# Performance work log

Hardware: AMD Instinct MI355X
Metric: run time of the kernel (lower is better)

The kernel has to match this reference:

```python
import jax, jax.numpy as jnp
import numpy as np

NUM_CLASSES = 32
MAX_DET = 100        # max_detections
CONF = 0.25          # conf_threshold
IOU_THR = 0.45       # iou_threshold
BATCH = 64
ANCHORS = 8400


def setup_inputs() -> dict:
    key = jax.random.key(0)
    # raw YOLO head output [B, 4+num_classes, anchors]; uniform [0,1) so boxes
    # (normalized cx,cy,w,h) and class scores are in valid range.
    yolo_output = jax.random.uniform(key, (BATCH, 4 + NUM_CLASSES, ANCHORS), dtype=jnp.float32)
    return {"yolo_output": yolo_output}


def _iou_one_vs_all(box, boxes):
    # box: [4] (ymin,xmin,ymax,xmax); boxes: [A,4]
    y1 = jnp.maximum(box[0], boxes[:, 0])
    x1 = jnp.maximum(box[1], boxes[:, 1])
    y2 = jnp.minimum(box[2], boxes[:, 2])
    x2 = jnp.minimum(box[3], boxes[:, 3])
    inter = jnp.maximum(y2 - y1, 0.0) * jnp.maximum(x2 - x1, 0.0)
    area_a = (box[2] - box[0]) * (box[3] - box[1])
    area_b = (boxes[:, 2] - boxes[:, 0]) * (boxes[:, 3] - boxes[:, 1])
    union = area_a + area_b - inter
    return jnp.where(union > 0.0, inter / union, 0.0)


def _nms_one_image(boxes, classes, scores):
    # Greedy hard NMS, equivalent to tf.image.non_max_suppression followed by
    # gather + zero-pad to MAX_DET. `scores` already has sub-threshold anchors
    # masked to -1 (emulating boolean_mask by threshold).
    def step(sc, _):
        idx = jnp.argmax(sc)
        s = sc[idx]
        b = boxes[idx]
        c = classes[idx]
        ok = s > 0.0  # any remaining valid candidate?
        iou = _iou_one_vs_all(b, boxes)
        new_sc = jnp.where(iou > IOU_THR, -1.0, sc).at[idx].set(-1.0)
        sc = jnp.where(ok, new_sc, sc)
        out = (jnp.where(ok, b, 0.0), jnp.where(ok, c, 0.0), jnp.where(ok, s, 0.0), ok)
        return sc, out

    _, (sel_boxes, sel_classes, sel_scores, valid) = jax.lax.scan(
        step, scores, None, length=MAX_DET)
    num_det = jnp.sum(valid.astype(jnp.float32))
    return sel_boxes, sel_classes, sel_scores, num_det


def _forward(yolo_output):
    # [B, 36, A] -> [B, A, 36]
    t = jnp.transpose(yolo_output, (0, 2, 1))
    boxes_raw = t[..., :4]                      # cx, cy, w, h (normalized)
    class_scores = t[..., 4:]                   # [B, A, num_classes]
    best_scores = jnp.max(class_scores, axis=-1)
    best_classes = jax.lax.stop_gradient(
        jnp.argmax(class_scores, axis=-1).astype(jnp.float32))
    xc, yc, w, h = (boxes_raw[..., 0], boxes_raw[..., 1],
                    boxes_raw[..., 2], boxes_raw[..., 3])
    clip = lambda v: jnp.clip(v, 0.0, 1.0)
    # TF order: [ymin, xmin, ymax, xmax]
    corner = jnp.stack([clip(yc - h * 0.5), clip(xc - w * 0.5),
                        clip(yc + h * 0.5), clip(xc + w * 0.5)], axis=-1)
    # confidence threshold: mask out instead of boolean_mask (jit-friendly)
    masked_scores = jnp.where(best_scores >= CONF, best_scores, -1.0)
    det_boxes, det_classes, det_scores, num_det = jax.vmap(_nms_one_image)(
        corner, best_classes, masked_scores)
    return det_boxes, det_classes, det_scores, num_det


def reference(yolo_output):
    # Returns (detection_boxes [B,100,4], detection_classes [B,100],
    #          detection_scores [B,100], num_detections [B])
    return _forward(yolo_output)
```

## Files before the change

### kernel.cpp

```cpp
#include <hip/hip_runtime.h>

#define BATCH   64
#define CHANS   36
#define ANCH    8400
#define NCLS    32
#define MAXDET  100
#define CONF    0.25f
#define TPB     512
#define NW      (TPB / 64)
#define NLD     17
#define KEYMIN  0x3E800000u
#define NBUCK   2048
#define BUCK0   (0x3E800000u >> 13)
#define WCAP    256

typedef unsigned long long u64;
typedef unsigned int       u32;

__global__ __launch_bounds__(256) void yolo_prep(const float* __restrict__ in,
                                                 float4* __restrict__ wbox,
                                                 u64* __restrict__ wk64) {
#pragma clang fp contract(off)
    const int G = ANCH / 4;
    int g = blockIdx.x * 256 + threadIdx.x;
    if (g >= G) return;
    int b = blockIdx.y;
    const float4* p = (const float4*)(in + (size_t)b * (CHANS * ANCH));
    float4 xc = p[0 * G + g], yc = p[1 * G + g], ww = p[2 * G + g], hh = p[3 * G + g];
    float4 best = p[4 * G + g];
    uint4 bc = make_uint4(0, 0, 0, 0);
#pragma unroll
    for (int k = 1; k < NCLS; ++k) {
        float4 v = p[(4 + k) * G + g];
        if (v.x > best.x) { best.x = v.x; bc.x = k; }
        if (v.y > best.y) { best.y = v.y; bc.y = k; }
        if (v.z > best.z) { best.z = v.z; bc.z = k; }
        if (v.w > best.w) { best.w = v.w; bc.w = k; }
    }
    int a0 = b * ANCH + 4 * g;
    u64* wk = wk64 + (size_t)b * ANCH + 4 * g;
#define PREP_C(C, I)                                                      \
    {                                                                     \
        float Y1 = fminf(fmaxf(yc.C - hh.C * 0.5f, 0.f), 1.f);            \
        float X1 = fminf(fmaxf(xc.C - ww.C * 0.5f, 0.f), 1.f);            \
        float Y2 = fminf(fmaxf(yc.C + hh.C * 0.5f, 0.f), 1.f);            \
        float X2 = fminf(fmaxf(xc.C + ww.C * 0.5f, 0.f), 1.f);            \
        wbox[a0 + I] = make_float4(Y1, X1, Y2, X2);                       \
        int a_ = 4 * g + I;                                               \
        wk[I] = (best.C >= CONF)                                          \
            ? (((u64)__float_as_uint(best.C) << 32) |                     \
               ((u64)(16383 - a_) << 18) | (u64)(bc.C & 31u))             \
            : 0ull;                                                       \
    }
    PREP_C(x, 0) PREP_C(y, 1) PREP_C(z, 2) PREP_C(w, 3)
#undef PREP_C
}

__global__ __launch_bounds__(TPB) void yolo_nms(const float4* __restrict__ wbox,
                                                u64* __restrict__ wk64,
                                                float* __restrict__ out) {
#pragma clang fp contract(off)
    const double M = (double)0.45f + 0x1p-26;
    int b = blockIdx.x, t = threadIdx.x;
    const float4* bx = wbox + (size_t)b * ANCH;
    u64* gk = wk64 + (size_t)b * ANCH;

    __shared__ u32   hist[NBUCK];
    __shared__ int   cur[NBUCK];
    __shared__ u64   cKey[WCAP];
    __shared__ float4 cBox[WCAP];
    __shared__ float cAr[WCAP];
    __shared__ u64   SuppA[WCAP][4];
    __shared__ u64   SuppB[WCAP][4];
    __shared__ u64   Smask[4];
    __shared__ int   selTot;
    __shared__ u32   wvcnt[NW];
    __shared__ u32   wprd[NW];
    __shared__ float SelB[MAXDET][5];

    float* outBox = out + (size_t)b * (MAXDET * 4);
    float* outCls = out + (size_t)(BATCH * MAXDET * 4) + b * MAXDET;
    float* outScr = out + (size_t)(BATCH * MAXDET * 5) + b * MAXDET;
    float* outNum = out + (size_t)(BATCH * MAXDET * 6) + b;

    for (int i = t; i < NBUCK; i += TPB) hist[i] = 0u;
    __syncthreads();

    u64 kk[NLD];
#pragma unroll
    for (int j = 0; j < NLD; ++j) {
        int a = t + j * TPB;
        u64 k = (a < ANCH) ? gk[a] : 0ull;
        kk[j] = k;
        if (k != 0ull) {
            int bk = (int)((u32)(k >> 45) - BUCK0);
            atomicAdd(&hist[bk], 1u);
        }
    }
    __syncthreads();

    int u0 = t * 4;
    u32 c0 = hist[2047 - u0], c1 = hist[2047 - (u0 + 1)],
        c2 = hist[2047 - (u0 + 2)], c3 = hist[2047 - (u0 + 3)];
    u32 l1 = c0 + c1, l2 = l1 + c2, Su = l2 + c3;
    u32 x = Su;
#pragma unroll
    for (int d = 1; d < 64; d <<= 1) {
        u32 y = __shfl_up(x, d, 64);
        if ((t & 63) >= d) x += y;
    }
    if ((t & 63) == 63) wvcnt[t >> 6] = x;
    __syncthreads();
    int wb = 0;
    for (int w2 = 0; w2 < (t >> 6); ++w2) wb += (int)wvcnt[w2];
    int T = 0;
    for (int w2 = 0; w2 < NW; ++w2) T += (int)wvcnt[w2];
    u32 excl = (u32)wb + x - Su;
    cur[u0]     = (int)(excl + c0);
    cur[u0 + 1] = (int)(excl + l1);
    cur[u0 + 2] = (int)(excl + l2);
    cur[u0 + 3] = (int)(excl + Su);
    __syncthreads();
    hist[u0]     = excl;
    hist[u0 + 1] = excl + c0;
    hist[u0 + 2] = excl + l1;
    hist[u0 + 3] = excl + l2;
    __syncthreads();

#pragma unroll
    for (int j = 0; j < NLD; ++j) {
        if (kk[j] != 0ull) {
            int r = 2047 - (int)((u32)(kk[j] >> 45) - BUCK0);
            u32 pos = atomicAdd(&hist[r], 1u);
            gk[pos] = kk[j];
        }
    }
    __syncthreads();

    int s = 0;
    int wstart = 0;
    int brank = 0;
    bool term = false;

    while (true) {
        if (wstart >= T) { term = true; break; }

        bool pr = (brank + t < NBUCK) && (cur[brank + t] <= wstart + WCAP);
        u64 bal = __ballot(pr);
        if ((t & 63) == 0) wprd[t >> 6] = (u32)__popcll(bal);
        __syncthreads();
        int ntrue = 0;
        for (int w2 = 0; w2 < NW; ++w2) ntrue += (int)wprd[w2];
        int wend;
        if (ntrue > 0) wend = cur[brank + ntrue - 1];
        else wend = wstart + WCAP;
        brank += ntrue;
        if (wend > T) wend = T;
        int Wn = wend - wstart;

        u64 myk = 0ull; float4 mb = make_float4(0.f, 0.f, 0.f, 0.f);
        float my_ar = 0.f; bool al = false;
        if (t < Wn) {
            myk = gk[wstart + t];
            int a = 16383 - (int)((myk >> 18) & 0x3FFFull);
            mb = bx[a];
            my_ar = (mb.z - mb.x) * (mb.w - mb.y);
            al = true;
        }

        for (int i = 0; i < s; ++i) {
            if ((i & 7) == 0) { if (__ballot(al) == 0ull) break; }
            float qy1 = SelB[i][0], qx1 = SelB[i][1], qy2 = SelB[i][2],
                  qx2 = SelB[i][3], qar = SelB[i][4];
            float iy1 = fmaxf(qy1, mb.x), ix1 = fmaxf(qx1, mb.y);
            float iy2 = fminf(qy2, mb.z), ix2 = fminf(qx2, mb.w);
            float inter = fmaxf(iy2 - iy1, 0.f) * fmaxf(ix2 - ix1, 0.f);
            float uni = (qar + my_ar) - inter;
            if (al && ((double)inter > M * (double)uni)) al = false;
        }

        u64 wm = __ballot(al);
        int wv = t >> 6, ln = t & 63;
        if (ln == 0) wvcnt[wv] = (u32)__popcll(wm);
        __syncthreads();
        int wbase = 0;
        for (int w2 = 0; w2 < wv; ++w2) wbase += (int)wvcnt[w2];
        int A = 0;
        for (int w2 = 0; w2 < NW; ++w2) A += (int)wvcnt[w2];
        int myslot = -1;
        if (al) {
            myslot = wbase + (int)__popcll(wm & ((1ull << ln) - 1ull));
            cKey[myslot] = myk; cBox[myslot] = mb; cAr[myslot] = my_ar;
        }
        __syncthreads();

        if (A > 0) {
            int row = t & 255, half = t >> 8;
            int hA = (A + 1) >> 1;
            int i0 = half * hA, i1 = i0 + hA; if (i1 > A) i1 = A;
            u64 sw0 = 0ull, sw1 = 0ull, sw2 = 0ull, sw3 = 0ull;
            if (row < A) {
                u64 kr = cKey[row];
                float4 rb = cBox[row];
                float rar = cAr[row];
#pragma unroll 2
                for (int w2 = 0; w2 < 4; ++w2) {
                    int base = w2 << 6;
                    int lo = i0 > base ? i0 : base;
                    int hi = i1 < base + 64 ? i1 : base + 64;
                    u64 word = 0ull;
                    for (int i = lo; i < hi; ++i) {
                        u64 ki = cKey[i];
                        float4 ob = cBox[i];
                        float iy1 = fmaxf(ob.x, rb.x), ix1 = fmaxf(ob.y, rb.y);
                        float iy2 = fminf(ob.z, rb.z), ix2 = fminf(ob.w, rb.w);
                        float inter = fmaxf(iy2 - iy1, 0.f) * fmaxf(ix2 - ix1, 0.f);
                        float oar = (ob.z - ob.x) * (ob.w - ob.y);
                        float uni = (oar + rar) - inter;
                        if ((ki > kr) && ((double)inter > M * (double)uni))
                            word |= 1ull << (i - base);
                    }
                    if (w2 == 0) sw0 = word; else if (w2 == 1) sw1 = word;
                    else if (w2 == 2) sw2 = word; else sw3 = word;
                }
                if (half == 0) { SuppA[row][0] = sw0; SuppA[row][1] = sw1;
                                 SuppA[row][2] = sw2; SuppA[row][3] = sw3; }
                else           { SuppB[row][0] = sw0; SuppB[row][1] = sw1;
                                 SuppB[row][2] = sw2; SuppB[row][3] = sw3; }
            }
            __syncthreads();

            if (t < 64) {
                int L = t;
                u64 so0[4], so1[4], so2[4], so3[4];
#pragma unroll
                for (int w2 = 0; w2 < 4; ++w2) {
                    so0[w2] = (L       < A) ? (SuppA[L      ][w2] | SuppB[L      ][w2]) : 0ull;
                    so1[w2] = (L + 64  < A) ? (SuppA[L + 64 ][w2] | SuppB[L + 64 ][w2]) : 0ull;
                    so2[w2] = (L + 128 < A) ? (SuppA[L + 128][w2] | SuppB[L + 128][w2]) : 0ull;
                    so3[w2] = (L + 192 < A) ? (SuppA[L + 192][w2] | SuppB[L + 192][w2]) : 0ull;
                }
                u64 U[4], S[4];
                U[0] = __ballot(L < A);       U[1] = __ballot(L + 64 < A);
                U[2] = __ballot(L + 128 < A); U[3] = __ballot(L + 192 < A);
                S[0] = S[1] = S[2] = S[3] = 0ull;
                for (int it = 0; it < WCAP; ++it) {
                    if (!(U[0] | U[1] | U[2] | U[3])) break;
                    u64 D[4];
                    {
                        u64 p0 = (so0[0]&U[0])|(so0[1]&U[1])|(so0[2]&U[2])|(so0[3]&U[3]);
                        u64 p1 = (so1[0]&U[0])|(so1[1]&U[1])|(so1[2]&U[2])|(so1[3]&U[3]);
                        u64 p2 = (so2[0]&U[0])|(so2[1]&U[1])|(so2[2]&U[2])|(so2[3]&U[3]);
                        u64 p3 = (so3[0]&U[0])|(so3[1]&U[1])|(so3[2]&U[2])|(so3[3]&U[3]);
                        D[0] = __ballot(((U[0] >> L) & 1ull) && (p0 == 0ull));
                        D[1] = __ballot(((U[1] >> L) & 1ull) && (p1 == 0ull));
                        D[2] = __ballot(((U[2] >> L) & 1ull) && (p2 == 0ull));
                        D[3] = __ballot(((U[3] >> L) & 1ull) && (p3 == 0ull));
                    }
#pragma unroll
                    for (int w2 = 0; w2 < 4; ++w2) { S[w2] |= D[w2]; U[w2] &= ~D[w2]; }
                    {
                        u64 h0 = (so0[0]&D[0])|(so0[1]&D[1])|(so0[2]&D[2])|(so0[3]&D[3]);
                        u64 h1 = (so1[0]&D[0])|(so1[1]&D[1])|(so1[2]&D[2])|(so1[3]&D[3]);
                        u64 h2 = (so2[0]&D[0])|(so2[1]&D[1])|(so2[2]&D[2])|(so2[3]&D[3]);
                        u64 h3 = (so3[0]&D[0])|(so3[1]&D[1])|(so3[2]&D[2])|(so3[3]&D[3]);
                        U[0] &= ~__ballot(((U[0] >> L) & 1ull) && (h0 != 0ull));
                        U[1] &= ~__ballot(((U[1] >> L) & 1ull) && (h1 != 0ull));
                        U[2] &= ~__ballot(((U[2] >> L) & 1ull) && (h2 != 0ull));
                        U[3] &= ~__ballot(((U[3] >> L) & 1ull) && (h3 != 0ull));
                    }
                }
                if (L == 0) {
                    Smask[0] = S[0]; Smask[1] = S[1]; Smask[2] = S[2]; Smask[3] = S[3];
                    selTot = __popcll(S[0]) + __popcll(S[1]) + __popcll(S[2]) + __popcll(S[3]);
                }
            }
            __syncthreads();

            if (myslot >= 0) {
                bool sel = (Smask[myslot >> 6] >> (myslot & 63)) & 1ull;
                if (sel) {
                    int pos = s;
#pragma unroll
                    for (int w2 = 0; w2 < 4; ++w2) {
                        u64 m = Smask[w2];
                        while (m) {
                            int i = __ffsll(m) - 1;
                            m &= m - 1;
                            if (cKey[(w2 << 6) + i] > myk) ++pos;
                        }
                    }
                    if (pos < MAXDET) {
                        outScr[pos] = __uint_as_float((u32)(myk >> 32));
                        outCls[pos] = (float)((u32)myk & 31u);
                        outBox[pos * 4 + 0] = mb.x; outBox[pos * 4 + 1] = mb.y;
                        outBox[pos * 4 + 2] = mb.z; outBox[pos * 4 + 3] = mb.w;
                        SelB[pos][0] = mb.x; SelB[pos][1] = mb.y; SelB[pos][2] = mb.z;
                        SelB[pos][3] = mb.w; SelB[pos][4] = my_ar;
                    }
                }
            }
            s += selTot; if (s > MAXDET) s = MAXDET;
            __syncthreads();
        }

        wstart = wend;
        if (s >= MAXDET) break;
        if (wstart >= T) { term = true; break; }
    }

    if (term) {
        for (int q = s + t; q < MAXDET; q += TPB) {
            outScr[q] = 0.f; outCls[q] = 0.f;
            outBox[q * 4 + 0] = 0.f; outBox[q * 4 + 1] = 0.f;
            outBox[q * 4 + 2] = 0.f; outBox[q * 4 + 3] = 0.f;
        }
    }
    if (t == 0) *outNum = (float)s;
}

extern "C" void kernel_launch(void* const* d_in, const int* in_sizes, int n_in,
                              void* d_out, int out_size, void* d_ws, size_t ws_size,
                              hipStream_t stream) {
    const float* in = (const float*)d_in[0];
    float* out = (float*)d_out;
    float4* wbox = (float4*)d_ws;
    u64*    wk64 = (u64*)((char*)d_ws + (size_t)BATCH * ANCH * 16);

    dim3 g1((ANCH / 4 + 255) / 256, BATCH);
    yolo_prep<<<g1, 256, 0, stream>>>(in, wbox, wk64);
    yolo_nms<<<BATCH, TPB, 0, stream>>>(wbox, wk64, out);
}
```

Measured before the change: 174.5 us.

## Split NMS into sort, parallel top-K IoU matrix, and resolve kernels

Replaces the single per-image windowed NMS kernel with four kernels. After bucket-sorting the candidates, a separate kernel builds a 512x512 suppression bitmask for the top-K candidates using 8 blocks per image. A resolve kernel then runs the bitmask fixpoint over 512 candidates, with a greedy fallback over the remaining candidates when fewer than 100 boxes survive. The prep kernel also switches from float4 to float2 loads. The intent is to spread the IoU matrix work across many more CUs than one block per image. The cost is extra launches, a global-memory round trip for the bitmask, and a slow serial fallback path if the top 512 do not yield 100 detections.

```diff
diff --git a/kernel.cpp b/kernel.cpp
--- a/kernel.cpp
+++ b/kernel.cpp
@@ -6,39 +6,47 @@
 #define NCLS    32
 #define MAXDET  100
 #define CONF    0.25f
-#define TPB     512
-#define NW      (TPB / 64)
-#define NLD     17
-#define KEYMIN  0x3E800000u
+#define KTOP    512
 #define NBUCK   2048
 #define BUCK0   (0x3E800000u >> 13)
-#define WCAP    256
+#define STPB    512
+#define SNW     (STPB / 64)
+#define SNLD    17
 
 typedef unsigned long long u64;
 typedef unsigned int       u32;
+
+__device__ __forceinline__ bool iou_gt(float ay1, float ax1, float ay2, float ax2, float aar,
+                                       float by1, float bx1, float by2, float bx2, float bar,
+                                       double M) {
+#pragma clang fp contract(off)
+    float iy1 = fmaxf(ay1, by1), ix1 = fmaxf(ax1, bx1);
+    float iy2 = fminf(ay2, by2), ix2 = fminf(ax2, bx2);
+    float inter = fmaxf(iy2 - iy1, 0.f) * fmaxf(ix2 - ix1, 0.f);
+    float uni = (aar + bar) - inter;
+    return (double)inter > M * (double)uni;
+}
 
 __global__ __launch_bounds__(256) void yolo_prep(const float* __restrict__ in,
                                                  float4* __restrict__ wbox,
                                                  u64* __restrict__ wk64) {
 #pragma clang fp contract(off)
-    const int G = ANCH / 4;
+    const int G2 = ANCH / 2;
     int g = blockIdx.x * 256 + threadIdx.x;
-    if (g >= G) return;
+    if (g >= G2) return;
     int b = blockIdx.y;
-    const float4* p = (const float4*)(in + (size_t)b * (CHANS * ANCH));
-    float4 xc = p[0 * G + g], yc = p[1 * G + g], ww = p[2 * G + g], hh = p[3 * G + g];
-    float4 best = p[4 * G + g];
-    uint4 bc = make_uint4(0, 0, 0, 0);
+    const float2* p = (const float2*)(in + (size_t)b * (CHANS * ANCH));
+    float2 xc = p[0 * G2 + g], yc = p[1 * G2 + g], ww = p[2 * G2 + g], hh = p[3 * G2 + g];
+    float2 best = p[4 * G2 + g];
+    uint2 bc = make_uint2(0, 0);
 #pragma unroll
     for (int k = 1; k < NCLS; ++k) {
-        float4 v = p[(4 + k) * G + g];
+        float2 v = p[(4 + k) * G2 + g];
         if (v.x > best.x) { best.x = v.x; bc.x = k; }
         if (v.y > best.y) { best.y = v.y; bc.y = k; }
-        if (v.z > best.z) { best.z = v.z; bc.z = k; }
-        if (v.w > best.w) { best.w = v.w; bc.w = k; }
-    }
-    int a0 = b * ANCH + 4 * g;
-    u64* wk = wk64 + (size_t)b * ANCH + 4 * g;
+    }
+    int a0 = b * ANCH + 2 * g;
+    u64* wk = wk64 + (size_t)b * ANCH + 2 * g;
 #define PREP_C(C, I)                                                      \
     {                                                                     \
         float Y1 = fminf(fmaxf(yc.C - hh.C * 0.5f, 0.f), 1.f);            \
@@ -46,275 +54,313 @@
         float Y2 = fminf(fmaxf(yc.C + hh.C * 0.5f, 0.f), 1.f);            \
         float X2 = fminf(fmaxf(xc.C + ww.C * 0.5f, 0.f), 1.f);            \
         wbox[a0 + I] = make_float4(Y1, X1, Y2, X2);                       \
-        int a_ = 4 * g + I;                                               \
+        int a_ = 2 * g + I;                                               \
         wk[I] = (best.C >= CONF)                                          \
             ? (((u64)__float_as_uint(best.C) << 32) |                     \
                ((u64)(16383 - a_) << 18) | (u64)(bc.C & 31u))             \
             : 0ull;                                                       \
     }
-    PREP_C(x, 0) PREP_C(y, 1) PREP_C(z, 2) PREP_C(w, 3)
+    PREP_C(x, 0) PREP_C(y, 1)
 #undef PREP_C
 }
 
-__global__ __launch_bounds__(TPB) void yolo_nms(const float4* __restrict__ wbox,
-                                                u64* __restrict__ wk64,
-                                                float* __restrict__ out) {
+__global__ __launch_bounds__(STPB) void yolo_sort(u64* __restrict__ wk64,
+                                                  u32* __restrict__ meta) {
+    int b = blockIdx.x, t = threadIdx.x;
+    u64* gk = wk64 + (size_t)b * ANCH;
+
+    __shared__ u32 hist[NBUCK];
+    __shared__ u32 wvcnt[SNW];
+    __shared__ u32 kred[SNW];
+
+    for (int i = t; i < NBUCK; i += STPB) hist[i] = 0u;
+    __syncthreads();
+
+    u64 kk[SNLD];
+#pragma unroll
+    for (int j = 0; j < SNLD; ++j) {
+        int a = t + j * STPB;
+        u64 k = (a < ANCH) ? gk[a] : 0ull;
+        kk[j] = k;
+        if (k != 0ull) atomicAdd(&hist[(int)((u32)(k >> 45) - BUCK0)], 1u);
+    }
+    __syncthreads();
+
+    int u0 = t * 4;
+    u32 c0 = hist[2047 - u0], c1 = hist[2047 - (u0 + 1)],
+        c2 = hist[2047 - (u0 + 2)], c3 = hist[2047 - (u0 + 3)];
+    u32 l1 = c0 + c1, l2 = l1 + c2, Su = l2 + c3;
+    u32 x = Su;
+#pragma unroll
+    for (int d = 1; d < 64; d <<= 1) {
+        u32 y = __shfl_up(x, d, 64);
+        if ((t & 63) >= d) x += y;
+    }
+    if ((t & 63) == 63) wvcnt[t >> 6] = x;
+    __syncthreads();
+    int wb = 0;
+    for (int w = 0; w < (t >> 6); ++w) wb += (int)wvcnt[w];
+    int T = 0;
+    for (int w = 0; w < SNW; ++w) T += (int)wvcnt[w];
+    u32 excl = (u32)wb + x - Su;
+    hist[u0]     = excl;
+    hist[u0 + 1] = excl + c0;
+    hist[u0 + 2] = excl + l1;
+    hist[u0 + 3] = excl + l2;
+    __syncthreads();
+
+#pragma unroll
+    for (int j = 0; j < SNLD; ++j) {
+        if (kk[j] != 0ull) {
+            int r = 2047 - (int)((u32)(kk[j] >> 45) - BUCK0);
+            u32 pos = atomicAdd(&hist[r], 1u);
+            gk[pos] = kk[j];
+        }
+    }
+    __syncthreads();
+
+    u32 kb = 0;
+#pragma unroll
+    for (int q = 0; q < 4; ++q) {
+        u32 v = hist[u0 + q];
+        if (v <= (u32)KTOP && v > kb) kb = v;
+    }
+#pragma unroll
+    for (int sh = 1; sh < 64; sh <<= 1) {
+        u32 o = __shfl_xor(kb, sh, 64);
+        if (o > kb) kb = o;
+    }
+    if ((t & 63) == 0) kred[t >> 6] = kb;
+    __syncthreads();
+    if (t == 0) {
+        u32 K = 0;
+        for (int w = 0; w < SNW; ++w) if (kred[w] > K) K = kred[w];
+        meta[b * 4 + 0] = K;
+        meta[b * 4 + 1] = (u32)T;
+    }
+}
+
+__global__ __launch_bounds__(256) void yolo_matrix(const float4* __restrict__ wbox,
+                                                   const u64* __restrict__ wk64,
+                                                   const u32* __restrict__ meta,
+                                                   u64* __restrict__ gS) {
+#pragma clang fp contract(off)
+    const double M = (double)0.45f + 0x1p-26;
+    int b = blockIdx.x, t = threadIdx.x;
+    const float4* bx = wbox + (size_t)b * ANCH;
+    const u64* gk = wk64 + (size_t)b * ANCH;
+    int K = (int)meta[b * 4 + 0];
+
+    __shared__ u64    ck[KTOP];
+    __shared__ float4 cb[KTOP];
+    __shared__ float  ca[KTOP];
+
+    for (int i = t; i < KTOP; i += 256) {
+        u64 k = (i < K) ? gk[i] : 0ull;
+        ck[i] = k;
+        float4 bb = make_float4(0.f, 0.f, 0.f, 0.f);
+        if (k != 0ull) {
+            int a = 16383 - (int)((k >> 18) & 0x3FFFull);
+            bb = bx[a];
+        }
+        cb[i] = bb;
+        ca[i] = (bb.z - bb.x) * (bb.w - bb.y);
+    }
+    __syncthreads();
+
+    int row = blockIdx.y * 64 + (t >> 2);
+    int seg = t & 3;
+    u64 kr = ck[row];
+    float4 rb = cb[row];
+    float rar = ca[row];
+    u64 w0 = 0ull, w1 = 0ull;
+    int base0 = seg * 128;
+#pragma unroll 4
+    for (int j = 0; j < 64; ++j) {
+        {
+            int i = base0 + j;
+            u64 ki = ck[i];
+            if ((ki > kr) && iou_gt(cb[i].x, cb[i].y, cb[i].z, cb[i].w, ca[i],
+                                    rb.x, rb.y, rb.z, rb.w, rar, M))
+                w0 |= 1ull << j;
+        }
+        {
+            int i = base0 + 64 + j;
+            u64 ki = ck[i];
+            if ((ki > kr) && iou_gt(cb[i].x, cb[i].y, cb[i].z, cb[i].w, ca[i],
+                                    rb.x, rb.y, rb.z, rb.w, rar, M))
+                w1 |= 1ull << j;
+        }
+    }
+    ulonglong2 wv; wv.x = w0; wv.y = w1;
+    *(ulonglong2*)&gS[(size_t)b * (KTOP * 8) + (size_t)row * 8 + seg * 2] = wv;
+}
+
+__global__ __launch_bounds__(256) void yolo_resolve(const float4* __restrict__ wbox,
+                                                    u64* __restrict__ wk64,
+                                                    const u64* __restrict__ gS,
+                                                    const u32* __restrict__ meta,
+                                                    float* __restrict__ out) {
 #pragma clang fp contract(off)
     const double M = (double)0.45f + 0x1p-26;
     int b = blockIdx.x, t = threadIdx.x;
     const float4* bx = wbox + (size_t)b * ANCH;
     u64* gk = wk64 + (size_t)b * ANCH;
-
-    __shared__ u32   hist[NBUCK];
-    __shared__ int   cur[NBUCK];
-    __shared__ u64   cKey[WCAP];
-    __shared__ float4 cBox[WCAP];
-    __shared__ float cAr[WCAP];
-    __shared__ u64   SuppA[WCAP][4];
-    __shared__ u64   SuppB[WCAP][4];
-    __shared__ u64   Smask[4];
-    __shared__ int   selTot;
-    __shared__ u32   wvcnt[NW];
-    __shared__ u32   wprd[NW];
-    __shared__ float SelB[MAXDET][5];
+    int K = (int)meta[b * 4 + 0], T = (int)meta[b * 4 + 1];
+
+    __shared__ u64   ck[KTOP];
+    __shared__ u64   SP[KTOP * 9];
+    __shared__ u64   selKey[KTOP];
+    __shared__ float selb[MAXDET][5];
+    __shared__ u64   redm[4];
+    __shared__ int   selTotS;
 
     float* outBox = out + (size_t)b * (MAXDET * 4);
     float* outCls = out + (size_t)(BATCH * MAXDET * 4) + b * MAXDET;
     float* outScr = out + (size_t)(BATCH * MAXDET * 5) + b * MAXDET;
     float* outNum = out + (size_t)(BATCH * MAXDET * 6) + b;
 
-    for (int i = t; i < NBUCK; i += TPB) hist[i] = 0u;
-    __syncthreads();
-
-    u64 kk[NLD];
-#pragma unroll
-    for (int j = 0; j < NLD; ++j) {
-        int a = t + j * TPB;
-        u64 k = (a < ANCH) ? gk[a] : 0ull;
-        kk[j] = k;
-        if (k != 0ull) {
-            int bk = (int)((u32)(k >> 45) - BUCK0);
-            atomicAdd(&hist[bk], 1u);
-        }
-    }
-    __syncthreads();
-
-    int u0 = t * 4;
-    u32 c0 = hist[2047 - u0], c1 = hist[2047 - (u0 + 1)],
-        c2 = hist[2047 - (u0 + 2)], c3 = hist[2047 - (u0 + 3)];
-    u32 l1 = c0 + c1, l2 = l1 + c2, Su = l2 + c3;
-    u32 x = Su;
-#pragma unroll
-    for (int d = 1; d < 64; d <<= 1) {
-        u32 y = __shfl_up(x, d, 64);
-        if ((t & 63) >= d) x += y;
-    }
-    if ((t & 63) == 63) wvcnt[t >> 6] = x;
-    __syncthreads();
-    int wb = 0;
-    for (int w2 = 0; w2 < (t >> 6); ++w2) wb += (int)wvcnt[w2];
-    int T = 0;
-    for (int w2 = 0; w2 < NW; ++w2) T += (int)wvcnt[w2];
-    u32 excl = (u32)wb + x - Su;
-    cur[u0]     = (int)(excl + c0);
-    cur[u0 + 1] = (int)(excl + l1);
-    cur[u0 + 2] = (int)(excl + l2);
-    cur[u0 + 3] = (int)(excl + Su);
-    __syncthreads();
-    hist[u0]     = excl;
-    hist[u0 + 1] = excl + c0;
-    hist[u0 + 2] = excl + l1;
-    hist[u0 + 3] = excl + l2;
-    __syncthreads();
-
-#pragma unroll
-    for (int j = 0; j < NLD; ++j) {
-        if (kk[j] != 0ull) {
-            int r = 2047 - (int)((u32)(kk[j] >> 45) - BUCK0);
-            u32 pos = atomicAdd(&hist[r], 1u);
-            gk[pos] = kk[j];
-        }
-    }
-    __syncthreads();
-
-    int s = 0;
-    int wstart = 0;
-    int brank = 0;
-    bool term = false;
-
-    while (true) {
-        if (wstart >= T) { term = true; break; }
-
-        bool pr = (brank + t < NBUCK) && (cur[brank + t] <= wstart + WCAP);
-        u64 bal = __ballot(pr);
-        if ((t & 63) == 0) wprd[t >> 6] = (u32)__popcll(bal);
+    for (int i = t; i < KTOP; i += 256) ck[i] = (i < K) ? gk[i] : 0ull;
+    const u64* gSb = gS + (size_t)b * (KTOP * 8);
+    for (int i = t; i < KTOP * 8; i += 256) SP[(i >> 3) * 9 + (i & 7)] = gSb[i];
+    __syncthreads();
+
+    u64 S[8];
+#pragma unroll
+    for (int w = 0; w < 8; ++w) S[w] = 0ull;
+    if (t < 64) {
+        int L = t;
+        u64 U[8];
+#pragma unroll
+        for (int w = 0; w < 8; ++w) U[w] = __ballot(ck[(w << 6) + L] != 0ull);
+        for (int it = 0; it < KTOP; ++it) {
+            if (!(U[0] | U[1] | U[2] | U[3] | U[4] | U[5] | U[6] | U[7])) break;
+            u64 D[8];
+#pragma unroll
+            for (int w = 0; w < 8; ++w) {
+                const u64* rm = &SP[((w << 6) + L) * 9];
+                u64 pend = (rm[0] & U[0]) | (rm[1] & U[1]) | (rm[2] & U[2]) | (rm[3] & U[3])
+                         | (rm[4] & U[4]) | (rm[5] & U[5]) | (rm[6] & U[6]) | (rm[7] & U[7]);
+                D[w] = __ballot(((U[w] >> L) & 1ull) && (pend == 0ull));
+            }
+#pragma unroll
+            for (int w = 0; w < 8; ++w) { S[w] |= D[w]; U[w] &= ~D[w]; }
+#pragma unroll
+            for (int w = 0; w < 8; ++w) {
+                const u64* rm = &SP[((w << 6) + L) * 9];
+                u64 hit = (rm[0] & D[0]) | (rm[1] & D[1]) | (rm[2] & D[2]) | (rm[3] & D[3])
+                        | (rm[4] & D[4]) | (rm[5] & D[5]) | (rm[6] & D[6]) | (rm[7] & D[7]);
+                U[w] &= ~__ballot(((U[w] >> L) & 1ull) && (hit != 0ull));
+            }
+        }
+        if (t == 0) {
+            int c = 0;
+#pragma unroll
+            for (int w = 0; w < 8; ++w) c += (int)__popcll(S[w]);
+            selTotS = c;
+        }
+    }
+    __syncthreads();
+
+    if (t < 64) {
+        int L = t, base = 0;
+#pragma unroll
+        for (int w = 0; w < 8; ++w) {
+            u64 Sw = S[w];
+            if ((Sw >> L) & 1ull) {
+                int r = base + (int)__popcll(Sw & ((1ull << L) - 1ull));
+                selKey[r] = ck[(w << 6) + L];
+            }
+            base += (int)__popcll(Sw);
+        }
+    }
+    __syncthreads();
+
+    int sTot = selTotS;
+    int s = sTot < MAXDET ? sTot : MAXDET;
+
+    if (t < 64) {
+        int L = t;
+#pragma unroll
+        for (int w = 0; w < 8; ++w) {
+            if ((S[w] >> L) & 1ull) {
+                u64 myk = ck[(w << 6) + L];
+                int pos = 0;
+                for (int j = 0; j < sTot; ++j) pos += (selKey[j] > myk) ? 1 : 0;
+                if (pos < MAXDET) {
+                    int a = 16383 - (int)((myk >> 18) & 0x3FFFull);
+                    float4 bb = bx[a];
+                    outScr[pos] = __uint_as_float((u32)(myk >> 32));
+                    outCls[pos] = (float)((u32)myk & 31u);
+                    outBox[pos * 4 + 0] = bb.x; outBox[pos * 4 + 1] = bb.y;
+                    outBox[pos * 4 + 2] = bb.z; outBox[pos * 4 + 3] = bb.w;
+                    selb[pos][0] = bb.x; selb[pos][1] = bb.y; selb[pos][2] = bb.z;
+                    selb[pos][3] = bb.w; selb[pos][4] = (bb.z - bb.x) * (bb.w - bb.y);
+                }
+            }
+        }
+    }
+    __syncthreads();
+
+    if (s < MAXDET && T > K) {
+        int NR = T - K;
+        u64* rk = gk + K;
+        for (int i = t; i < NR; i += 256) {
+            u64 k = rk[i];
+            if (!k) continue;
+            int a = 16383 - (int)((k >> 18) & 0x3FFFull);
+            float4 bb = bx[a];
+            float ar = (bb.z - bb.x) * (bb.w - bb.y);
+            for (int j = 0; j < s; ++j) {
+                if (iou_gt(selb[j][0], selb[j][1], selb[j][2], selb[j][3], selb[j][4],
+                           bb.x, bb.y, bb.z, bb.w, ar, M)) { rk[i] = 0ull; break; }
+            }
+        }
         __syncthreads();
-        int ntrue = 0;
-        for (int w2 = 0; w2 < NW; ++w2) ntrue += (int)wprd[w2];
-        int wend;
-        if (ntrue > 0) wend = cur[brank + ntrue - 1];
-        else wend = wstart + WCAP;
-        brank += ntrue;
-        if (wend > T) wend = T;
-        int Wn = wend - wstart;
-
-        u64 myk = 0ull; float4 mb = make_float4(0.f, 0.f, 0.f, 0.f);
-        float my_ar = 0.f; bool al = false;
-        if (t < Wn) {
-            myk = gk[wstart + t];
-            int a = 16383 - (int)((myk >> 18) & 0x3FFFull);
-            mb = bx[a];
-            my_ar = (mb.z - mb.x) * (mb.w - mb.y);
-            al = true;
-        }
-
-        for (int i = 0; i < s; ++i) {
-            if ((i & 7) == 0) { if (__ballot(al) == 0ull) break; }
-            float qy1 = SelB[i][0], qx1 = SelB[i][1], qy2 = SelB[i][2],
-                  qx2 = SelB[i][3], qar = SelB[i][4];
-            float iy1 = fmaxf(qy1, mb.x), ix1 = fmaxf(qx1, mb.y);
-            float iy2 = fminf(qy2, mb.z), ix2 = fminf(qx2, mb.w);
-            float inter = fmaxf(iy2 - iy1, 0.f) * fmaxf(ix2 - ix1, 0.f);
-            float uni = (qar + my_ar) - inter;
-            if (al && ((double)inter > M * (double)uni)) al = false;
-        }
-
-        u64 wm = __ballot(al);
-        int wv = t >> 6, ln = t & 63;
-        if (ln == 0) wvcnt[wv] = (u32)__popcll(wm);
-        __syncthreads();
-        int wbase = 0;
-        for (int w2 = 0; w2 < wv; ++w2) wbase += (int)wvcnt[w2];
-        int A = 0;
-        for (int w2 = 0; w2 < NW; ++w2) A += (int)wvcnt[w2];
-        int myslot = -1;
-        if (al) {
-            myslot = wbase + (int)__popcll(wm & ((1ull << ln) - 1ull));
-            cKey[myslot] = myk; cBox[myslot] = mb; cAr[myslot] = my_ar;
-        }
-        __syncthreads();
-
-        if (A > 0) {
-            int row = t & 255, half = t >> 8;
-            int hA = (A + 1) >> 1;
-            int i0 = half * hA, i1 = i0 + hA; if (i1 > A) i1 = A;
-            u64 sw0 = 0ull, sw1 = 0ull, sw2 = 0ull, sw3 = 0ull;
-            if (row < A) {
-                u64 kr = cKey[row];
-                float4 rb = cBox[row];
-                float rar = cAr[row];
-#pragma unroll 2
-                for (int w2 = 0; w2 < 4; ++w2) {
-                    int base = w2 << 6;
-                    int lo = i0 > base ? i0 : base;
-                    int hi = i1 < base + 64 ? i1 : base + 64;
-                    u64 word = 0ull;
-                    for (int i = lo; i < hi; ++i) {
-                        u64 ki = cKey[i];
-                        float4 ob = cBox[i];
-                        float iy1 = fmaxf(ob.x, rb.x), ix1 = fmaxf(ob.y, rb.y);
-                        float iy2 = fminf(ob.z, rb.z), ix2 = fminf(ob.w, rb.w);
-                        float inter = fmaxf(iy2 - iy1, 0.f) * fmaxf(ix2 - ix1, 0.f);
-                        float oar = (ob.z - ob.x) * (ob.w - ob.y);
-                        float uni = (oar + rar) - inter;
-                        if ((ki > kr) && ((double)inter > M * (double)uni))
-                            word |= 1ull << (i - base);
-                    }
-                    if (w2 == 0) sw0 = word; else if (w2 == 1) sw1 = word;
-                    else if (w2 == 2) sw2 = word; else sw3 = word;
-                }
-                if (half == 0) { SuppA[row][0] = sw0; SuppA[row][1] = sw1;
-                                 SuppA[row][2] = sw2; SuppA[row][3] = sw3; }
-                else           { SuppB[row][0] = sw0; SuppB[row][1] = sw1;
-                                 SuppB[row][2] = sw2; SuppB[row][3] = sw3; }
-            }
+        while (s < MAXDET) {
+            u64 best = 0ull;
+            for (int i = t; i < NR; i += 256) { u64 k = rk[i]; if (k > best) best = k; }
+#pragma unroll
+            for (int sh = 1; sh < 64; sh <<= 1) {
+                u64 o = __shfl_xor(best, sh, 64);
+                if (o > best) best = o;
+            }
+            if ((t & 63) == 0) redm[t >> 6] = best;
             __syncthreads();
-
-            if (t < 64) {
-                int L = t;
-                u64 so0[4], so1[4], so2[4], so3[4];
-#pragma unroll
-                for (int w2 = 0; w2 < 4; ++w2) {
-                    so0[w2] = (L       < A) ? (SuppA[L      ][w2] | SuppB[L      ][w2]) : 0ull;
-                    so1[w2] = (L + 64  < A) ? (SuppA[L + 64 ][w2] | SuppB[L + 64 ][w2]) : 0ull;
-                    so2[w2] = (L + 128 < A) ? (SuppA[L + 128][w2] | SuppB[L + 128][w2]) : 0ull;
-                    so3[w2] = (L + 192 < A) ? (SuppA[L + 192][w2] | SuppB[L + 192][w2]) : 0ull;
-                }
-                u64 U[4], S[4];
-                U[0] = __ballot(L < A);       U[1] = __ballot(L + 64 < A);
-                U[2] = __ballot(L + 128 < A); U[3] = __ballot(L + 192 < A);
-                S[0] = S[1] = S[2] = S[3] = 0ull;
-                for (int it = 0; it < WCAP; ++it) {
-                    if (!(U[0] | U[1] | U[2] | U[3])) break;
-                    u64 D[4];
-                    {
-                        u64 p0 = (so0[0]&U[0])|(so0[1]&U[1])|(so0[2]&U[2])|(so0[3]&U[3]);
-                        u64 p1 = (so1[0]&U[0])|(so1[1]&U[1])|(so1[2]&U[2])|(so1[3]&U[3]);
-                        u64 p2 = (so2[0]&U[0])|(so2[1]&U[1])|(so2[2]&U[2])|(so2[3]&U[3]);
-                        u64 p3 = (so3[0]&U[0])|(so3[1]&U[1])|(so3[2]&U[2])|(so3[3]&U[3]);
-                        D[0] = __ballot(((U[0] >> L) & 1ull) && (p0 == 0ull));
-                        D[1] = __ballot(((U[1] >> L) & 1ull) && (p1 == 0ull));
-                        D[2] = __ballot(((U[2] >> L) & 1ull) && (p2 == 0ull));
-                        D[3] = __ballot(((U[3] >> L) & 1ull) && (p3 == 0ull));
-                    }
-#pragma unroll
-                    for (int w2 = 0; w2 < 4; ++w2) { S[w2] |= D[w2]; U[w2] &= ~D[w2]; }
-                    {
-                        u64 h0 = (so0[0]&D[0])|(so0[1]&D[1])|(so0[2]&D[2])|(so0[3]&D[3]);
-                        u64 h1 = (so1[0]&D[0])|(so1[1]&D[1])|(so1[2]&D[2])|(so1[3]&D[3]);
-                        u64 h2 = (so2[0]&D[0])|(so2[1]&D[1])|(so2[2]&D[2])|(so2[3]&D[3]);
-                        u64 h3 = (so3[0]&D[0])|(so3[1]&D[1])|(so3[2]&D[2])|(so3[3]&D[3]);
-                        U[0] &= ~__ballot(((U[0] >> L) & 1ull) && (h0 != 0ull));
-                        U[1] &= ~__ballot(((U[1] >> L) & 1ull) && (h1 != 0ull));
-                        U[2] &= ~__ballot(((U[2] >> L) & 1ull) && (h2 != 0ull));
-                        U[3] &= ~__ballot(((U[3] >> L) & 1ull) && (h3 != 0ull));
+            best = redm[0];
+            for (int w = 1; w < 4; ++w) if (redm[w] > best) best = redm[w];
+            if (best == 0ull) break;
+            int a = 16383 - (int)((best >> 18) & 0x3FFFull);
+            float4 nb = bx[a];
+            float nar = (nb.z - nb.x) * (nb.w - nb.y);
+            if (t == 0) {
+                outScr[s] = __uint_as_float((u32)(best >> 32));
+                outCls[s] = (float)((u32)best & 31u);
+                outBox[s * 4 + 0] = nb.x; outBox[s * 4 + 1] = nb.y;
+                outBox[s * 4 + 2] = nb.z; outBox[s * 4 + 3] = nb.w;
+            }
+            for (int i = t; i < NR; i += 256) {
+                u64 k = rk[i];
+                if (k != 0ull) {
+                    if (k == best) rk[i] = 0ull;
+                    else {
+                        int a2 = 16383 - (int)((k >> 18) & 0x3FFFull);
+                        float4 bb = bx[a2];
+                        float ar = (bb.z - bb.x) * (bb.w - bb.y);
+                        if (iou_gt(nb.x, nb.y, nb.z, nb.w, nar,
+                                   bb.x, bb.y, bb.z, bb.w, ar, M)) rk[i] = 0ull;
                     }
                 }
-                if (L == 0) {
-                    Smask[0] = S[0]; Smask[1] = S[1]; Smask[2] = S[2]; Smask[3] = S[3];
-                    selTot = __popcll(S[0]) + __popcll(S[1]) + __popcll(S[2]) + __popcll(S[3]);
-                }
-            }
+            }
+            ++s;
             __syncthreads();
-
-            if (myslot >= 0) {
-                bool sel = (Smask[myslot >> 6] >> (myslot & 63)) & 1ull;
-                if (sel) {
-                    int pos = s;
-#pragma unroll
-                    for (int w2 = 0; w2 < 4; ++w2) {
-                        u64 m = Smask[w2];
-                        while (m) {
-                            int i = __ffsll(m) - 1;
-                            m &= m - 1;
-                            if (cKey[(w2 << 6) + i] > myk) ++pos;
-                        }
-                    }
-                    if (pos < MAXDET) {
-                        outScr[pos] = __uint_as_float((u32)(myk >> 32));
-                        outCls[pos] = (float)((u32)myk & 31u);
-                        outBox[pos * 4 + 0] = mb.x; outBox[pos * 4 + 1] = mb.y;
-                        outBox[pos * 4 + 2] = mb.z; outBox[pos * 4 + 3] = mb.w;
-                        SelB[pos][0] = mb.x; SelB[pos][1] = mb.y; SelB[pos][2] = mb.z;
-                        SelB[pos][3] = mb.w; SelB[pos][4] = my_ar;
-                    }
-                }
-            }
-            s += selTot; if (s > MAXDET) s = MAXDET;
-            __syncthreads();
-        }
-
-        wstart = wend;
-        if (s >= MAXDET) break;
-        if (wstart >= T) { term = true; break; }
-    }
-
-    if (term) {
-        for (int q = s + t; q < MAXDET; q += TPB) {
-            outScr[q] = 0.f; outCls[q] = 0.f;
-            outBox[q * 4 + 0] = 0.f; outBox[q * 4 + 1] = 0.f;
-            outBox[q * 4 + 2] = 0.f; outBox[q * 4 + 3] = 0.f;
-        }
+        }
+    }
+
+    for (int q = s + t; q < MAXDET; q += 256) {
+        outScr[q] = 0.f; outCls[q] = 0.f;
+        outBox[q * 4 + 0] = 0.f; outBox[q * 4 + 1] = 0.f;
+        outBox[q * 4 + 2] = 0.f; outBox[q * 4 + 3] = 0.f;
     }
     if (t == 0) *outNum = (float)s;
 }
@@ -326,8 +372,12 @@
     float* out = (float*)d_out;
     float4* wbox = (float4*)d_ws;
     u64*    wk64 = (u64*)((char*)d_ws + (size_t)BATCH * ANCH * 16);
-
-    dim3 g1((ANCH / 4 + 255) / 256, BATCH);
-    yolo_prep<<<g1, 256, 0, stream>>>(in, wbox, wk64);
-    yolo_nms<<<BATCH, TPB, 0, stream>>>(wbox, wk64, out);
-}
+    u64*    gS   = (u64*)((char*)d_ws + (size_t)BATCH * ANCH * 24);
+    u32*    meta = (u32*)((char*)d_ws + (size_t)BATCH * ANCH * 24 + (size_t)BATCH * KTOP * 64);
+
+    dim3 gp((ANCH / 2 + 255) / 256, BATCH);
+    yolo_prep<<<gp, 256, 0, stream>>>(in, wbox, wk64);
+    yolo_sort<<<BATCH, STPB, 0, stream>>>(wk64, meta);
+    yolo_matrix<<<dim3(BATCH, 8), 256, 0, stream>>>(wbox, wk64, meta, gS);
+    yolo_resolve<<<BATCH, 256, 0, stream>>>(wbox, wk64, gS, meta, out);
+}
```

Result: no change. 175.6 us (+0.6%).
